# Optimization experiments

Hardware: AMD Instinct MI355X
Metric: run time of the kernel (lower is better)

The kernel has to match this reference:

```python
import jax, jax.numpy as jnp
import numpy as np

N = 250000   # total nodes
F = 256      # in_channels
G = 4096     # num graphs (size)
T = 6        # processing_steps


def setup_inputs() -> dict:
    key = jax.random.key(0)
    k1, k2, k3, k4, k5, k6 = jax.random.split(key, 6)
    x = jax.random.normal(k1, (N, F), dtype=jnp.float32)
    batch = jnp.sort(jax.random.randint(k2, (N,), 0, G, dtype=jnp.int32))
    s = 1.0 / np.sqrt(F)  # torch LSTM init: U(-1/sqrt(hidden), 1/sqrt(hidden))
    Wih = jax.random.uniform(k3, (4 * F, 2 * F), minval=-s, maxval=s, dtype=jnp.float32)
    Whh = jax.random.uniform(k4, (4 * F, F), minval=-s, maxval=s, dtype=jnp.float32)
    bih = jax.random.uniform(k5, (4 * F,), minval=-s, maxval=s, dtype=jnp.float32)
    bhh = jax.random.uniform(k6, (4 * F,), minval=-s, maxval=s, dtype=jnp.float32)
    return {"x": x, "batch": batch, "size": G, "Wih": Wih, "Whh": Whh, "bih": bih, "bhh": bhh}


def _set2set(x, batch, size, Wih, Whh, bih, bhh):
    Fdim = Whh.shape[1]
    h = jnp.zeros((size, Fdim), x.dtype)
    c = jnp.zeros((size, Fdim), x.dtype)
    q_star = jnp.zeros((size, 2 * Fdim), x.dtype)
    for _ in range(T):
        # single-layer LSTM step on [size, 2F] -> [size, F]; torch gate order i,f,g,o
        gates = q_star @ Wih.T + h @ Whh.T + (bih + bhh)
        i, f, g, o = jnp.split(gates, 4, axis=-1)
        c = jax.nn.sigmoid(f) * c + jax.nn.sigmoid(i) * jnp.tanh(g)
        h = jax.nn.sigmoid(o) * jnp.tanh(c)
        q = h  # [size, F]
        # content-based attention score per node
        e = jnp.sum(x * q[batch], axis=-1, keepdims=True)  # [N, 1]
        # segment softmax over nodes of each graph (PyG adds 1e-16 to denom)
        emax = jax.ops.segment_max(e, batch, num_segments=size)  # [size, 1]
        ex = jnp.exp(e - emax[batch])
        denom = jax.ops.segment_sum(ex, batch, num_segments=size)
        a = ex / (denom[batch] + 1e-16)
        # weighted scatter-add readout
        r = jax.ops.segment_sum(a * x, batch, num_segments=size)  # [size, F]
        q_star = jnp.concatenate([q, r], axis=-1)
    return q_star  # [size, 2F]


def reference(x, batch, size, Wih, Whh, bih, bhh):
    return _set2set(x, batch, size, Wih, Whh, bih, bhh)
```

## Files before the change

kernel.cpp:

```cpp
#include <hip/hip_runtime.h>
#include <cstdint>
#include <cstddef>

#define NN 250000
#define FF 256
#define GG 4096
#define TT 6
#define GPB 16
#define SBLK (GG / GPB)

typedef _Float16 half8_t __attribute__((ext_vector_type(8)));
typedef _Float16 half4_t __attribute__((ext_vector_type(4)));
typedef _Float16 half2_t __attribute__((ext_vector_type(2)));
typedef float f32x4 __attribute__((ext_vector_type(4)));

__device__ __forceinline__ float fdot2f(half2_t a, half2_t b, float c) {
#if __has_builtin(__builtin_amdgcn_fdot2)
  return __builtin_amdgcn_fdot2(a, b, c, false);
#else
  return c + (float)a[0] * (float)b[0] + (float)a[1] * (float)b[1];
#endif
}

__device__ __forceinline__ float dot8(half8_t x, half8_t q) {
  float d = fdot2f((half2_t){x[0], x[1]}, (half2_t){q[0], q[1]}, 0.f);
  d = fdot2f((half2_t){x[2], x[3]}, (half2_t){q[2], q[3]}, d);
  d = fdot2f((half2_t){x[4], x[5]}, (half2_t){q[4], q[5]}, d);
  d = fdot2f((half2_t){x[6], x[7]}, (half2_t){q[6], q[7]}, d);
  return d;
}

__global__ __launch_bounds__(256) void attn0_kernel(
    const float* __restrict__ x32, const int* __restrict__ batch,
    const float* __restrict__ Wih, const float* __restrict__ Whh,
    const float* __restrict__ bih, const float* __restrict__ bhh,
    _Float16* __restrict__ w16f, int* __restrict__ starts,
    _Float16* __restrict__ x16w, _Float16* __restrict__ q16out) {
  int g = blockIdx.x, tid = threadIdx.x, lane = tid & 63, w = tid >> 6;
  __shared__ int sgs[2];
  __shared__ __align__(16) float h_sh[FF];
  __shared__ __align__(16) float rw[4][FF];
  __shared__ float mw[4], sw[4];

  if (tid < 2) {
    int target = g + tid;
    int lo = 0;
    if (target >= GG) lo = NN;
    else {
      int hi = NN;
      while (lo < hi) {
        int mid = (lo + hi) >> 1;
        if (batch[mid] < target) lo = mid + 1; else hi = mid;
      }
    }
    sgs[tid] = lo;
    starts[g + tid] = lo;
  }

  if (g < 512) {
#pragma unroll
    for (int e = 0; e < 4; ++e) {
      int idx = g * 1024 + e * 256 + tid;
      int n = idx >> 9, k = idx & 511;
      float v = Wih[(size_t)n * 512 + k];
      if (k < FF) v += Whh[(size_t)n * FF + k];
      int dest = ((n >> 4) * 16 + (k >> 5)) * 512 + ((k >> 3) & 3) * 128 +
                 (n & 15) * 8 + (k & 7);
      w16f[dest] = (_Float16)v;
    }
  }

  float bi = bih[tid] + bhh[tid];
  float bg = bih[tid + 512] + bhh[tid + 512];
  float bo = bih[tid + 768] + bhh[tid + 768];
  float si0 = 1.f / (1.f + __expf(-bi));
  float so0 = 1.f / (1.f + __expf(-bo));
  float cv0 = si0 * tanhf(bg);
  float hv0 = so0 * tanhf(cv0);
  q16out[(size_t)g * 512 + tid] = (_Float16)hv0;
  h_sh[tid] = hv0;
  __syncthreads();

  f32x4 qv = *(const f32x4*)&h_sh[4 * lane];
  int s0 = sgs[0], cnt = sgs[1] - sgs[0];

  float m = -INFINITY, ssum = 0.f;
  f32x4 racc = {0.f, 0.f, 0.f, 0.f};
  for (int i0 = w * 4; i0 < cnt; i0 += 16) {
    f32x4 xv[4];
    float d[4];
    bool vld[4];
#pragma unroll
    for (int j = 0; j < 4; ++j) {
      int idx = i0 + j;
      vld[j] = idx < cnt;
      int node = vld[j] ? idx : cnt - 1;
      xv[j] = __builtin_nontemporal_load(
          (const f32x4*)(x32 + (size_t)(s0 + node) * FF + 4 * lane));
    }
#pragma unroll
    for (int j = 0; j < 4; ++j) {
      half4_t hx;
      hx[0] = (_Float16)xv[j][0]; hx[1] = (_Float16)xv[j][1];
      hx[2] = (_Float16)xv[j][2]; hx[3] = (_Float16)xv[j][3];
      int node = vld[j] ? (i0 + j) : cnt - 1;
      *(half4_t*)(x16w + (size_t)(s0 + node) * FF + 4 * lane) = hx;
    }
#pragma unroll
    for (int j = 0; j < 4; ++j)
      d[j] = xv[j][0] * qv[0] + xv[j][1] * qv[1] + xv[j][2] * qv[2] + xv[j][3] * qv[3];
#pragma unroll
    for (int off = 32; off; off >>= 1)
#pragma unroll
      for (int j = 0; j < 4; ++j) d[j] += __shfl_xor(d[j], off);
#pragma unroll
    for (int j = 0; j < 4; ++j) if (!vld[j]) d[j] = -INFINITY;
    float gm = fmaxf(fmaxf(d[0], d[1]), fmaxf(d[2], d[3]));
    if (gm > m) {
      float sc = __expf(m - gm);
      ssum *= sc; racc *= sc;
      m = gm;
    }
#pragma unroll
    for (int j = 0; j < 4; ++j) {
      float p = __expf(d[j] - m);
      ssum += p;
      racc += p * xv[j];
    }
  }

  if (lane == 0) { mw[w] = m; sw[w] = ssum; }
  *(f32x4*)&rw[w][4 * lane] = racc;
  __syncthreads();
  float M = fmaxf(fmaxf(mw[0], mw[1]), fmaxf(mw[2], mw[3]));
  float e0 = (mw[0] == -INFINITY) ? 0.f : __expf(mw[0] - M);
  float e1 = (mw[1] == -INFINITY) ? 0.f : __expf(mw[1] - M);
  float e2 = (mw[2] == -INFINITY) ? 0.f : __expf(mw[2] - M);
  float e3 = (mw[3] == -INFINITY) ? 0.f : __expf(mw[3] - M);
  float denom = sw[0] * e0 + sw[1] * e1 + sw[2] * e2 + sw[3] * e3;
  float rs = rw[0][tid] * e0 + rw[1][tid] * e1 + rw[2][tid] * e2 + rw[3][tid] * e3;
  float r = rs / (denom + 1e-16f);
  if (cnt == 0) r = 0.f;
  q16out[(size_t)g * 512 + FF + tid] = (_Float16)r;
}

__global__ __launch_bounds__(1024, 1) void steps_kernel(
    const _Float16* __restrict__ x16, const _Float16* __restrict__ w16f,
    const _Float16* __restrict__ q16a, const int* __restrict__ starts,
    const float* __restrict__ bih, const float* __restrict__ bhh,
    float* __restrict__ qstar) {
  int tid = threadIdx.x, lane = tid & 63, w = tid >> 6;
  int lr = lane & 15, kq = lane >> 4;
  int sl = lane & 31, hf = lane >> 5;
  int g0 = blockIdx.x * GPB;

  __shared__ _Float16 qs[GPB][520];
  __shared__ float cst[GPB][256];
  __shared__ int sgs[GPB + 1];

  if (tid <= GPB) sgs[tid] = starts[g0 + tid];
  {
    int i = tid >> 6, c8 = tid & 63;
    *(half8_t*)&qs[i][c8 * 8] =
        *(const half8_t*)(q16a + (size_t)(g0 + i) * 512 + c8 * 8);
  }
  {
    int f = tid & 255;
    float bi = bih[f] + bhh[f];
    float bg = bih[f + 512] + bhh[f + 512];
    float si0 = 1.f / (1.f + __expf(-bi));
    float cv0 = si0 * tanhf(bg);
    for (int i = tid >> 8; i < GPB; i += 4) cst[i][f] = cv0;
  }
  int f = w * 16 + lr;
  float bi_ = bih[f] + bhh[f];
  float bf_ = bih[f + 256] + bhh[f + 256];
  float bg_ = bih[f + 512] + bhh[f + 512];
  float bo_ = bih[f + 768] + bhh[f + 768];
  __syncthreads();

  for (int t = 1; t < TT; ++t) {
    bool last = (t == TT - 1);

    f32x4 acc[4];
#pragma unroll
    for (int gt = 0; gt < 4; ++gt) acc[gt] = (f32x4){0.f, 0.f, 0.f, 0.f};

#pragma unroll 4
    for (int ks = 0; ks < 16; ++ks) {
      int kk = ks * 32 + kq * 8;
      half8_t a = *(const half8_t*)&qs[lr][kk];
#pragma unroll
      for (int gt = 0; gt < 4; ++gt) {
        int nf = gt * 16 + w;
        half8_t b = *(const half8_t*)(
            w16f + ((size_t)nf * 16 + ks) * 512 + lane * 8);
        acc[gt] = __builtin_amdgcn_mfma_f32_16x16x32_f16(a, b, acc[gt], 0, 0, 0);
      }
    }
    __syncthreads();

#pragma unroll
    for (int r = 0; r < 4; ++r) {
      int gl = kq * 4 + r;
      float ig = acc[0][r] + bi_;
      float fg = acc[1][r] + bf_;
      float gv = acc[2][r] + bg_;
      float og = acc[3][r] + bo_;
      float si = 1.f / (1.f + __expf(-ig));
      float sf = 1.f / (1.f + __expf(-fg));
      float so = 1.f / (1.f + __expf(-og));
      float cv = sf * cst[gl][f] + si * tanhf(gv);
      float hv = so * tanhf(cv);
      cst[gl][f] = cv;
      qs[gl][f] = (_Float16)hv;
      if (last) qstar[(size_t)(g0 + gl) * 512 + f] = hv;
    }
    __syncthreads();

    {
      int ii = w;
      int s0 = sgs[ii];
      int cnt = sgs[ii + 1] - s0;
      half8_t qh = *(const half8_t*)&qs[ii][sl * 8];

      float m = -INFINITY, ssum = 0.f;
      float racc[8];
#pragma unroll
      for (int e = 0; e < 8; ++e) racc[e] = 0.f;

      for (int i0 = 0; i0 < cnt; i0 += 16) {
        half8_t hx[8];
        float d[8];
        bool vld[8];
#pragma unroll
        for (int j = 0; j < 8; ++j) {
          int idx = i0 + j * 2 + hf;
          vld[j] = idx < cnt;
          int node = vld[j] ? idx : cnt - 1;
          hx[j] = *(const half8_t*)(x16 + (size_t)(s0 + node) * FF + sl * 8);
        }
#pragma unroll
        for (int j = 0; j < 8; ++j) d[j] = dot8(hx[j], qh);
#pragma unroll
        for (int off = 1; off <= 16; off <<= 1)
#pragma unroll
          for (int j = 0; j < 8; ++j) d[j] += __shfl_xor(d[j], off);
#pragma unroll
        for (int j = 0; j < 8; ++j) if (!vld[j]) d[j] = -INFINITY;
        float gm = -INFINITY;
#pragma unroll
        for (int j = 0; j < 8; ++j) {
          float dother = __shfl_xor(d[j], 32);
          gm = fmaxf(gm, fmaxf(d[j], dother));
        }
        if (gm > m) {
          float sc = __expf(m - gm);
          ssum *= sc;
#pragma unroll
          for (int e = 0; e < 8; ++e) racc[e] *= sc;
          m = gm;
        }
#pragma unroll
        for (int j = 0; j < 8; ++j) {
          float p = __expf(d[j] - m);
          ssum += p;
#pragma unroll
          for (int e = 0; e < 8; ++e) racc[e] += p * (float)hx[j][e];
        }
      }

      ssum += __shfl_xor(ssum, 32);
#pragma unroll
      for (int e = 0; e < 8; ++e) racc[e] += __shfl_xor(racc[e], 32);
      float inv = 1.0f / (ssum + 1e-16f);

      if (hf == 0) {
        half8_t rh;
        float rv[8];
#pragma unroll
        for (int e = 0; e < 8; ++e) {
          rv[e] = (cnt == 0) ? 0.f : racc[e] * inv;
          rh[e] = (_Float16)rv[e];
        }
        *(half8_t*)&qs[ii][256 + sl * 8] = rh;
        if (last) {
          f32x4 lo = {rv[0], rv[1], rv[2], rv[3]};
          f32x4 hi = {rv[4], rv[5], rv[6], rv[7]};
          *(f32x4*)(qstar + (size_t)(g0 + ii) * 512 + 256 + sl * 8) = lo;
          *(f32x4*)(qstar + (size_t)(g0 + ii) * 512 + 260 + sl * 8) = hi;
        }
      }
    }
    __syncthreads();
  }
}

extern "C" void kernel_launch(void* const* d_in, const int* in_sizes, int n_in,
                              void* d_out, int out_size, void* d_ws, size_t ws_size,
                              hipStream_t stream) {
  const float* x   = (const float*)d_in[0];
  const int* batch = (const int*)d_in[1];
  const float* Wih = (const float*)d_in[3];
  const float* Whh = (const float*)d_in[4];
  const float* bih = (const float*)d_in[5];
  const float* bhh = (const float*)d_in[6];
  float* qstar = (float*)d_out;

  uint8_t* p = (uint8_t*)d_ws;
  auto alloc = [&](size_t bytes) {
    uint8_t* q = p;
    p += (bytes + 255) & ~(size_t)255;
    return q;
  };
  _Float16* q16a = (_Float16*)alloc((size_t)GG * 2 * FF * 2);
  _Float16* w16f = (_Float16*)alloc((size_t)4 * FF * 2 * FF * 2);
  int* starts    = (int*)alloc((size_t)(GG + 1) * 4);
  _Float16* x16  = (_Float16*)alloc((size_t)NN * FF * 2);

  attn0_kernel<<<GG, 256, 0, stream>>>(
      x, batch, Wih, Whh, bih, bhh, w16f, starts, x16, q16a);

  steps_kernel<<<SBLK, 1024, 0, stream>>>(
      x16, w16f, q16a, starts, bih, bhh, qstar);
}
```

Before: 246.7 us.

## Compute attention scores one node per lane, then accumulate readout in a second pass

Restructures the per-graph attention loop so each lane computes the full 256-wide dot product for its own node, which removes the per-node cross-lane shuffle reductions. Softmax weights are staged in a shared buffer, and a second pass re-reads the x rows with half-wave feature slices to accumulate the weighted readout. In exchange, x is read twice per step, the score loads are strided per lane (one row per lane, poorly coalesced), and the readout loop processes only two nodes per iteration with a data-dependent trip count.

Measured after the change: 536.7 us. +117.6%, slower.

```diff
diff --git a/kernel.cpp b/kernel.cpp
--- a/kernel.cpp
+++ b/kernel.cpp
@@ -22,12 +22,12 @@
 #endif
 }
 
-__device__ __forceinline__ float dot8(half8_t x, half8_t q) {
-  float d = fdot2f((half2_t){x[0], x[1]}, (half2_t){q[0], q[1]}, 0.f);
-  d = fdot2f((half2_t){x[2], x[3]}, (half2_t){q[2], q[3]}, d);
-  d = fdot2f((half2_t){x[4], x[5]}, (half2_t){q[4], q[5]}, d);
-  d = fdot2f((half2_t){x[6], x[7]}, (half2_t){q[6], q[7]}, d);
-  return d;
+__device__ __forceinline__ float dot8acc(half8_t x, half8_t q, float acc) {
+  acc = fdot2f((half2_t){x[0], x[1]}, (half2_t){q[0], q[1]}, acc);
+  acc = fdot2f((half2_t){x[2], x[3]}, (half2_t){q[2], q[3]}, acc);
+  acc = fdot2f((half2_t){x[4], x[5]}, (half2_t){q[4], q[5]}, acc);
+  acc = fdot2f((half2_t){x[6], x[7]}, (half2_t){q[6], q[7]}, acc);
+  return acc;
 }
 
 __global__ __launch_bounds__(256) void attn0_kernel(
@@ -156,6 +156,7 @@
 
   __shared__ _Float16 qs[GPB][520];
   __shared__ float cst[GPB][256];
+  __shared__ float pbuf[GPB][64];
   __shared__ int sgs[GPB + 1];
 
   if (tid <= GPB) sgs[tid] = starts[g0 + tid];
@@ -222,66 +223,76 @@
       int ii = w;
       int s0 = sgs[ii];
       int cnt = sgs[ii + 1] - s0;
-      half8_t qh = *(const half8_t*)&qs[ii][sl * 8];
 
       float m = -INFINITY, ssum = 0.f;
       float racc[8];
 #pragma unroll
       for (int e = 0; e < 8; ++e) racc[e] = 0.f;
 
-      for (int i0 = 0; i0 < cnt; i0 += 16) {
-        half8_t hx[8];
-        float d[8];
-        bool vld[8];
-#pragma unroll
-        for (int j = 0; j < 8; ++j) {
-          int idx = i0 + j * 2 + hf;
-          vld[j] = idx < cnt;
-          int node = vld[j] ? idx : cnt - 1;
-          hx[j] = *(const half8_t*)(x16 + (size_t)(s0 + node) * FF + sl * 8);
-        }
-#pragma unroll
-        for (int j = 0; j < 8; ++j) d[j] = dot8(hx[j], qh);
-#pragma unroll
-        for (int off = 1; off <= 16; off <<= 1)
-#pragma unroll
-          for (int j = 0; j < 8; ++j) d[j] += __shfl_xor(d[j], off);
-#pragma unroll
-        for (int j = 0; j < 8; ++j) if (!vld[j]) d[j] = -INFINITY;
-        float gm = -INFINITY;
-#pragma unroll
-        for (int j = 0; j < 8; ++j) {
-          float dother = __shfl_xor(d[j], 32);
-          gm = fmaxf(gm, fmaxf(d[j], dother));
-        }
-        if (gm > m) {
-          float sc = __expf(m - gm);
+      for (int base = 0; base < cnt; base += 64) {
+        int node = base + lane;
+        bool v = node < cnt;
+        const _Float16* row = x16 + (size_t)(s0 + (v ? node : cnt - 1)) * FF;
+        float d0 = 0.f, d1 = 0.f, d2 = 0.f, d3 = 0.f;
+#pragma unroll
+        for (int c = 0; c < 32; c += 4) {
+          half8_t x0 = *(const half8_t*)(row + (c + 0) * 8);
+          half8_t x1 = *(const half8_t*)(row + (c + 1) * 8);
+          half8_t x2 = *(const half8_t*)(row + (c + 2) * 8);
+          half8_t x3 = *(const half8_t*)(row + (c + 3) * 8);
+          half8_t q0 = *(const half8_t*)&qs[ii][(c + 0) * 8];
+          half8_t q1 = *(const half8_t*)&qs[ii][(c + 1) * 8];
+          half8_t q2 = *(const half8_t*)&qs[ii][(c + 2) * 8];
+          half8_t q3 = *(const half8_t*)&qs[ii][(c + 3) * 8];
+          d0 = dot8acc(x0, q0, d0);
+          d1 = dot8acc(x1, q1, d1);
+          d2 = dot8acc(x2, q2, d2);
+          d3 = dot8acc(x3, q3, d3);
+        }
+        float e = (d0 + d1) + (d2 + d3);
+        if (!v) e = -INFINITY;
+
+        float cm = e;
+#pragma unroll
+        for (int off = 32; off; off >>= 1) cm = fmaxf(cm, __shfl_xor(cm, off));
+        if (cm > m) {
+          float sc = __expf(m - cm);
           ssum *= sc;
 #pragma unroll
-          for (int e = 0; e < 8; ++e) racc[e] *= sc;
-          m = gm;
-        }
-#pragma unroll
-        for (int j = 0; j < 8; ++j) {
-          float p = __expf(d[j] - m);
-          ssum += p;
-#pragma unroll
-          for (int e = 0; e < 8; ++e) racc[e] += p * (float)hx[j][e];
+          for (int e2 = 0; e2 < 8; ++e2) racc[e2] *= sc;
+          m = cm;
+        }
+        float p = __expf(e - m);
+        float cs = p;
+#pragma unroll
+        for (int off = 32; off; off >>= 1) cs += __shfl_xor(cs, off);
+        ssum += cs;
+        pbuf[ii][lane] = p;
+
+        int lim = cnt - base; if (lim > 64) lim = 64;
+        for (int i = 0; i < lim; i += 2) {
+          int j = i + hf;
+          bool jv = j < lim;
+          float pj = pbuf[ii][jv ? j : 0];
+          if (!jv) pj = 0.f;
+          half8_t hx = *(const half8_t*)(
+              x16 + (size_t)(s0 + base + (jv ? j : 0)) * FF + sl * 8);
+#pragma unroll
+          for (int e2 = 0; e2 < 8; ++e2) racc[e2] += pj * (float)hx[e2];
         }
       }
 
-      ssum += __shfl_xor(ssum, 32);
-#pragma unroll
-      for (int e = 0; e < 8; ++e) racc[e] += __shfl_xor(racc[e], 32);
+#pragma unroll
+      for (int e2 = 0; e2 < 8; ++e2) racc[e2] += __shfl_xor(racc[e2], 32);
       float inv = 1.0f / (ssum + 1e-16f);
 
       if (hf == 0) {
         half8_t rh;
         float rv[8];
 #pragma unroll
-        for (int e = 0; e < 8; ++e) {
-          rv[e] = (cnt == 0) ? 0.f : racc[e] * inv;
-          rh[e] = (_Float16)rv[e];
+        for (int e2 = 0; e2 < 8; ++e2) {
+          rv[e2] = (cnt == 0) ? 0.f : racc[e2] * inv;
+          rh[e2] = (_Float16)rv[e2];
         }
         *(half8_t*)&qs[ii][256 + sl * 8] = rh;
         if (last) {
```

## Halve graphs per block and split each graph's attention across two waves

Applied to the files above, without the earlier changes.

Reduces graphs per block from 16 to 8, doubling the grid, and assigns two wavefronts per graph in the attention phase, each handling alternate 16-node chunks. The partial max, sum and readout vectors are merged through shared memory with an extra barrier. The LSTM MFMA still computes 16 rows, with the upper 8 zero-padded and discarded, so gate compute and weight loads per useful graph double. The goal is more parallelism across CUs for the memory-bound node scan, at the cost of redundant matmul work and an extra sync.

New measurement: 408.6 us. 65.7% more time.

```diff
diff --git a/kernel.cpp b/kernel.cpp
--- a/kernel.cpp
+++ b/kernel.cpp
@@ -6,7 +6,7 @@
 #define FF 256
 #define GG 4096
 #define TT 6
-#define GPB 16
+#define GPB 8
 #define SBLK (GG / GPB)
 
 typedef _Float16 half8_t __attribute__((ext_vector_type(8)));
@@ -144,7 +144,7 @@
   q16out[(size_t)g * 512 + FF + tid] = (_Float16)r;
 }
 
-__global__ __launch_bounds__(1024, 1) void steps_kernel(
+__global__ __launch_bounds__(1024, 8) void steps_kernel(
     const _Float16* __restrict__ x16, const _Float16* __restrict__ w16f,
     const _Float16* __restrict__ q16a, const int* __restrict__ starts,
     const float* __restrict__ bih, const float* __restrict__ bhh,
@@ -154,15 +154,20 @@
   int sl = lane & 31, hf = lane >> 5;
   int g0 = blockIdx.x * GPB;
 
-  __shared__ _Float16 qs[GPB][520];
+  __shared__ _Float16 qs[16][520];
   __shared__ float cst[GPB][256];
+  __shared__ float rw[GPB][2][256];
+  __shared__ float mw[GPB][2], sw[GPB][2];
   __shared__ int sgs[GPB + 1];
 
   if (tid <= GPB) sgs[tid] = starts[g0 + tid];
   {
     int i = tid >> 6, c8 = tid & 63;
-    *(half8_t*)&qs[i][c8 * 8] =
-        *(const half8_t*)(q16a + (size_t)(g0 + i) * 512 + c8 * 8);
+    if (i < GPB)
+      *(half8_t*)&qs[i][c8 * 8] =
+          *(const half8_t*)(q16a + (size_t)(g0 + i) * 512 + c8 * 8);
+    else
+      *(half8_t*)&qs[i][c8 * 8] = (half8_t){0, 0, 0, 0, 0, 0, 0, 0};
   }
   {
     int f = tid & 255;
@@ -203,23 +208,25 @@
 #pragma unroll
     for (int r = 0; r < 4; ++r) {
       int gl = kq * 4 + r;
-      float ig = acc[0][r] + bi_;
-      float fg = acc[1][r] + bf_;
-      float gv = acc[2][r] + bg_;
-      float og = acc[3][r] + bo_;
-      float si = 1.f / (1.f + __expf(-ig));
-      float sf = 1.f / (1.f + __expf(-fg));
-      float so = 1.f / (1.f + __expf(-og));
-      float cv = sf * cst[gl][f] + si * tanhf(gv);
-      float hv = so * tanhf(cv);
-      cst[gl][f] = cv;
-      qs[gl][f] = (_Float16)hv;
-      if (last) qstar[(size_t)(g0 + gl) * 512 + f] = hv;
+      if (gl < GPB) {
+        float ig = acc[0][r] + bi_;
+        float fg = acc[1][r] + bf_;
+        float gv = acc[2][r] + bg_;
+        float og = acc[3][r] + bo_;
+        float si = 1.f / (1.f + __expf(-ig));
+        float sf = 1.f / (1.f + __expf(-fg));
+        float so = 1.f / (1.f + __expf(-og));
+        float cv = sf * cst[gl][f] + si * tanhf(gv);
+        float hv = so * tanhf(cv);
+        cst[gl][f] = cv;
+        qs[gl][f] = (_Float16)hv;
+        if (last) qstar[(size_t)(g0 + gl) * 512 + f] = hv;
+      }
     }
     __syncthreads();
 
     {
-      int ii = w;
+      int ii = w >> 1, pp = w & 1;
       int s0 = sgs[ii];
       int cnt = sgs[ii + 1] - s0;
       half8_t qh = *(const half8_t*)&qs[ii][sl * 8];
@@ -229,7 +236,7 @@
 #pragma unroll
       for (int e = 0; e < 8; ++e) racc[e] = 0.f;
 
-      for (int i0 = 0; i0 < cnt; i0 += 16) {
+      for (int i0 = pp * 16; i0 < cnt; i0 += 32) {
         half8_t hx[8];
         float d[8];
         bool vld[8];
@@ -273,15 +280,33 @@
       ssum += __shfl_xor(ssum, 32);
 #pragma unroll
       for (int e = 0; e < 8; ++e) racc[e] += __shfl_xor(racc[e], 32);
-      float inv = 1.0f / (ssum + 1e-16f);
-
+
+      if (lane == 0) { mw[ii][pp] = m; sw[ii][pp] = ssum; }
+      if (hf == 0) {
+#pragma unroll
+        for (int e = 0; e < 8; ++e) rw[ii][pp][sl * 8 + e] = racc[e];
+      }
+    }
+    __syncthreads();
+
+    if ((w & 1) == 0) {
+      int ii = w >> 1;
+      int cnt = sgs[ii + 1] - sgs[ii];
+      float m0 = mw[ii][0], m1 = mw[ii][1];
+      float M = fmaxf(m0, m1);
+      float e0 = (m0 == -INFINITY) ? 0.f : __expf(m0 - M);
+      float e1 = (m1 == -INFINITY) ? 0.f : __expf(m1 - M);
+      float denom = sw[ii][0] * e0 + sw[ii][1] * e1;
+      float inv = 1.0f / (denom + 1e-16f);
       if (hf == 0) {
         half8_t rh;
         float rv[8];
 #pragma unroll
         for (int e = 0; e < 8; ++e) {
-          rv[e] = (cnt == 0) ? 0.f : racc[e] * inv;
-          rh[e] = (_Float16)rv[e];
+          float v = (rw[ii][0][sl * 8 + e] * e0 + rw[ii][1][sl * 8 + e] * e1) * inv;
+          if (cnt == 0) v = 0.f;
+          rv[e] = v;
+          rh[e] = (_Float16)v;
         }
         *(half8_t*)&qs[ii][256 + sl * 8] = rh;
         if (last) {
```
